# Performance work log

Measured on AMD Instinct MI355X. Metric: run time of the kernel, lower is better.

The kernel has to match this reference:

```python
import jax, jax.numpy as jnp
import numpy as np

W_L1, W_NORMAL, W_LAPLACIAN = 1.0, 1.0, 0.1
NORM_EPS = 1e-6   # F.normalize eps
COS_EPS = 1e-8    # F.cosine_similarity default eps


def setup_inputs() -> dict:
    key = jax.random.key(0)
    k1, k2, k3, k4, k5, k6 = jax.random.split(key, 6)
    N, F, NNZ = 1_000_000, 2_000_000, 8_000_000
    return {
        "V_rec": jax.random.normal(k1, (N, 3), dtype=jnp.float32),
        "V_gt": jax.random.normal(k2, (N, 3), dtype=jnp.float32),
        "faces": jax.random.randint(k3, (F, 3), 0, N, dtype=jnp.int64)
        if jax.config.jax_enable_x64 else jax.random.randint(k3, (F, 3), 0, N, dtype=jnp.int32),
        "L_rows": jax.random.randint(k4, (NNZ,), 0, N, dtype=jnp.int32),
        "L_cols": jax.random.randint(k5, (NNZ,), 0, N, dtype=jnp.int32),
        "L_vals": jax.random.normal(k6, (NNZ,), dtype=jnp.float32),
    }


def _vertex_normals(verts, faces):
    # gather verts by face indices: [F,3] each
    v0 = verts[faces[:, 0]]
    v1 = verts[faces[:, 1]]
    v2 = verts[faces[:, 2]]
    face_normals = jnp.cross(v1 - v0, v2 - v0)  # [F,3]
    vn = (jnp.zeros_like(verts)
          .at[faces[:, 0]].add(face_normals)
          .at[faces[:, 1]].add(face_normals)
          .at[faces[:, 2]].add(face_normals))
    norm = jnp.linalg.norm(vn, axis=1, keepdims=True)
    return vn / jnp.maximum(norm, NORM_EPS)


def _cosine_sim(a, b):
    dot = jnp.sum(a * b, axis=1)
    na = jnp.linalg.norm(a, axis=1)
    nb = jnp.linalg.norm(b, axis=1)
    return dot / (jnp.maximum(na, COS_EPS) * jnp.maximum(nb, COS_EPS))


def _spmm(rows, cols, vals, V):
    # sparse [N,N] @ dense [N,3] via gather + segment_sum
    return jax.ops.segment_sum(vals[:, None] * V[cols], rows, num_segments=V.shape[0])


def reference(V_rec, V_gt, faces, L_rows, L_cols, L_vals):
    # L1 term
    loss_l1 = jnp.mean(jnp.abs(V_rec - V_gt))
    # Normal cosine term
    normals_gt = _vertex_normals(V_gt, faces)
    normals_rec = _vertex_normals(V_rec, faces)
    cos_n = jnp.nan_to_num(_cosine_sim(normals_rec, normals_gt), nan=1.0)
    loss_normal = jnp.mean(1.0 - cos_n)
    # Laplacian cosine term
    delta_gt = _spmm(L_rows, L_cols, L_vals, V_gt)
    delta_rec = _spmm(L_rows, L_cols, L_vals, V_rec)
    cos_l = jnp.nan_to_num(_cosine_sim(delta_rec, delta_gt), nan=1.0)
    loss_laplacian = jnp.mean(1.0 - cos_l)
    finite = jnp.isfinite(delta_gt).all() & jnp.isfinite(delta_rec).all()
    loss_laplacian = jnp.where(finite, loss_laplacian, 0.0)
    return W_L1 * loss_l1 + W_NORMAL * loss_normal + W_LAPLACIAN * loss_laplacian
```

## Files before the change

### kernel.cpp

```cpp
#include <hip/hip_runtime.h>
#include <hip/hip_bf16.h>

#define NORM_EPS_F 1e-6f
#define COS_EPS_F  1e-8f
#define BK   512
#define BKSH 9
#define NBGMAX 2048
#define CHF1 2048
#define CHL1 4096
#define K2   32
#define NOCT 8

__device__ __forceinline__ void atomAddF(float* p, float v) {
    unsafeAtomicAdd(p, v);
}

template<int NV>
__device__ __forceinline__ void blockReduceAtomicN(float (&v)[NV], float* dst) {
    #pragma unroll
    for (int off = 32; off > 0; off >>= 1) {
        #pragma unroll
        for (int k = 0; k < NV; ++k) v[k] += __shfl_down(v[k], off, 64);
    }
    __shared__ float red[4][NV];
    int wave = threadIdx.x >> 6, lane = threadIdx.x & 63;
    if (lane == 0) {
        #pragma unroll
        for (int k = 0; k < NV; ++k) red[wave][k] = v[k];
    }
    __syncthreads();
    if (threadIdx.x == 0) {
        float s[NV];
        #pragma unroll
        for (int k = 0; k < NV; ++k) s[k] = 0.f;
        for (int w = 0; w < 4; ++w)
            #pragma unroll
            for (int k = 0; k < NV; ++k) s[k] += red[w][k];
        #pragma unroll
        for (int k = 0; k < NV; ++k) atomAddF(&dst[k], s[k]);
    }
}


__global__ void __launch_bounds__(256) pack_l1_kernel(
    const float* __restrict__ Vr, const float* __restrict__ Vg,
    float4* __restrict__ Vp, float* __restrict__ accum, int N)
{
    int i = blockIdx.x * blockDim.x + threadIdx.x;
    float l1[1] = {0.f};
    if (i < N) {
        float rx = Vr[3 * i], ry = Vr[3 * i + 1], rz = Vr[3 * i + 2];
        float gx = Vg[3 * i], gy = Vg[3 * i + 1], gz = Vg[3 * i + 2];
        Vp[2 * i]     = make_float4(rx, ry, rz, 0.f);
        Vp[2 * i + 1] = make_float4(gx, gy, gz, 0.f);
        l1[0] = fabsf(rx - gx) + fabsf(ry - gy) + fabsf(rz - gz);
    }
    blockReduceAtomicN<1>(l1, &accum[0]);
}

__global__ void __launch_bounds__(256) fn_kernel(
    const float4* __restrict__ Vp, const int* __restrict__ faces,
    float4* __restrict__ FN, int F)
{
    int half = (F + 1) >> 1;
    int t = blockIdx.x * blockDim.x + threadIdx.x;
    if (t >= half) return;
    int fi[2] = {t, t + half};
    int n = (fi[1] < F) ? 2 : 1;
    int idx[2][3];
    #pragma unroll
    for (int k = 0; k < 2; ++k) if (k < n) {
        idx[k][0] = faces[3 * fi[k]];
        idx[k][1] = faces[3 * fi[k] + 1];
        idx[k][2] = faces[3 * fi[k] + 2];
    }
    float4 r0[2], r1[2], r2[2], g0[2], g1[2], g2[2];
    #pragma unroll
    for (int k = 0; k < 2; ++k) if (k < n) {
        r0[k] = Vp[2 * idx[k][0]]; g0[k] = Vp[2 * idx[k][0] + 1];
        r1[k] = Vp[2 * idx[k][1]]; g1[k] = Vp[2 * idx[k][1] + 1];
        r2[k] = Vp[2 * idx[k][2]]; g2[k] = Vp[2 * idx[k][2] + 1];
    }
    #pragma unroll
    for (int k = 0; k < 2; ++k) if (k < n) {
        float ax = r1[k].x - r0[k].x, ay = r1[k].y - r0[k].y, az = r1[k].z - r0[k].z;
        float bx = r2[k].x - r0[k].x, by = r2[k].y - r0[k].y, bz = r2[k].z - r0[k].z;
        FN[2 * fi[k]] = make_float4(ay * bz - az * by, az * bx - ax * bz, ax * by - ay * bx, 0.f);
        ax = g1[k].x - g0[k].x; ay = g1[k].y - g0[k].y; az = g1[k].z - g0[k].z;
        bx = g2[k].x - g0[k].x; by = g2[k].y - g0[k].y; bz = g2[k].z - g0[k].z;
        FN[2 * fi[k] + 1] = make_float4(ay * bz - az * by, az * bx - ax * bz, ax * by - ay * bx, 0.f);
    }
}


__global__ void __launch_bounds__(256) bucket_F1(
    const int* __restrict__ faces, int* __restrict__ cntC,
    unsigned* __restrict__ recA, unsigned char* __restrict__ recC,
    int capC, int F, int b0, int bcnt, int chunk)
{
    __shared__ int hist[64];
    int f0 = blockIdx.x * chunk, f1 = min(f0 + chunk, F);
    if (threadIdx.x < 64) hist[threadIdx.x] = 0;
    __syncthreads();
    for (int f = f0 + threadIdx.x; f < f1; f += 256) {
        #pragma unroll
        for (int c = 0; c < 3; ++c) {
            unsigned fb = ((unsigned)faces[3 * f + c] >> BKSH) - (unsigned)b0;
            if (fb < (unsigned)bcnt) atomicAdd(&hist[fb >> 5], 1);
        }
    }
    __syncthreads();
    if (threadIdx.x < 64) {
        int h = hist[threadIdx.x];
        if (h) hist[threadIdx.x] = atomicAdd(&cntC[threadIdx.x], h);
    }
    __syncthreads();
    for (int f = f0 + threadIdx.x; f < f1; f += 256) {
        #pragma unroll
        for (int c = 0; c < 3; ++c) {
            int v = faces[3 * f + c];
            unsigned fb = ((unsigned)v >> BKSH) - (unsigned)b0;
            if (fb < (unsigned)bcnt) {
                int pos = atomicAdd(&hist[fb >> 5], 1);
                if (pos < capC) {
                    size_t idx = (size_t)(fb >> 5) * capC + pos;
                    recA[idx] = ((unsigned)f << BKSH) | ((unsigned)v & (BK - 1));
                    recC[idx] = (unsigned char)(fb & 31);
                }
            }
        }
    }
}

__global__ void __launch_bounds__(256) bucket_L1(
    const int* __restrict__ rows, const int* __restrict__ cols,
    const float* __restrict__ vals, int* __restrict__ cntC,
    int2* __restrict__ recA, unsigned char* __restrict__ recC,
    int capC, int nnz, int b0, int bcnt, int chunk, int octsh)
{
    __shared__ int hist[64];
    int i0 = blockIdx.x * chunk, i1 = min(i0 + chunk, nnz);
    if (threadIdx.x < 64) hist[threadIdx.x] = 0;
    __syncthreads();
    for (int i = i0 + threadIdx.x; i < i1; i += 256) {
        unsigned fb = ((unsigned)rows[i] >> BKSH) - (unsigned)b0;
        if (fb < (unsigned)bcnt) atomicAdd(&hist[fb >> 5], 1);
    }
    __syncthreads();
    if (threadIdx.x < 64) {
        int h = hist[threadIdx.x];
        if (h) hist[threadIdx.x] = atomicAdd(&cntC[threadIdx.x], h);
    }
    __syncthreads();
    for (int i = i0 + threadIdx.x; i < i1; i += 256) {
        int r = rows[i];
        unsigned fb = ((unsigned)r >> BKSH) - (unsigned)b0;
        if (fb < (unsigned)bcnt) {
            int pos = atomicAdd(&hist[fb >> 5], 1);
            if (pos < capC) {
                size_t idx = (size_t)(fb >> 5) * capC + pos;
                unsigned c = (unsigned)cols[i];
                recA[idx] = make_int2(
                    (int)((c << BKSH) | ((unsigned)r & (BK - 1))),
                    __float_as_int(vals[i]));
                recC[idx] = (unsigned char)(((fb & 31) << 3) | (c >> octsh));
            }
        }
    }
}


__global__ void __launch_bounds__(256) bucket_F2(
    const int* __restrict__ cntC, const unsigned* __restrict__ recA,
    const unsigned char* __restrict__ recC, int capC,
    int* __restrict__ cntFine, unsigned* __restrict__ fine, int capF)
{
    __shared__ int hist[32];
    int c = blockIdx.x;
    int K = gridDim.y, k = blockIdx.y;
    int ch = (capC + K - 1) / K;
    int n = min(cntC[c], capC);
    int i0 = k * ch, i1 = min(i0 + ch, n);
    if (threadIdx.x < 32) hist[threadIdx.x] = 0;
    __syncthreads();
    const size_t base = (size_t)c * capC;
    for (int i = i0 + threadIdx.x; i < i1; i += 256)
        atomicAdd(&hist[recC[base + i]], 1);
    __syncthreads();
    if (threadIdx.x < 32) {
        int h = hist[threadIdx.x];
        if (h) hist[threadIdx.x] = atomicAdd(&cntFine[(c << 5) + threadIdx.x], h);
    }
    __syncthreads();
    for (int i = i0 + threadIdx.x; i < i1; i += 256) {
        int fic = recC[base + i];
        int pos = atomicAdd(&hist[fic], 1);
        if (pos < capF)
            fine[(size_t)((c << 5) + fic) * capF + pos] = recA[base + i];
    }
}

__global__ void __launch_bounds__(256) bucket_L2(
    const int* __restrict__ cntC, const int2* __restrict__ recA,
    const unsigned char* __restrict__ recC, int capC,
    int* __restrict__ cntFine, int2* __restrict__ fine, int capS)
{
    __shared__ int hist[256];
    int c = blockIdx.x;
    int K = gridDim.y, k = blockIdx.y;
    int ch = (capC + K - 1) / K;
    int n = min(cntC[c], capC);
    int i0 = k * ch, i1 = min(i0 + ch, n);
    hist[threadIdx.x] = 0;
    __syncthreads();
    const size_t base = (size_t)c * capC;
    for (int i = i0 + threadIdx.x; i < i1; i += 256)
        atomicAdd(&hist[recC[base + i]], 1);
    __syncthreads();
    {
        int h = hist[threadIdx.x];
        if (h) hist[threadIdx.x] = atomicAdd(&cntFine[(c << 8) + threadIdx.x], h);
    }
    __syncthreads();
    for (int i = i0 + threadIdx.x; i < i1; i += 256) {
        int fic = recC[base + i];
        int pos = atomicAdd(&hist[fic], 1);
        if (pos < capS)
            fine[(size_t)((c << 8) + fic) * capS + pos] = recA[base + i];
    }
}


__global__ void __launch_bounds__(256) accum_normals_kernel(
    const float4* __restrict__ Vp, const float4* __restrict__ FN,
    const int* __restrict__ faces,
    const int* __restrict__ cnt, const unsigned* __restrict__ recF, int capF,
    float* __restrict__ accum, int N, int b0, int use_fn)
{
    __shared__ float vnr[3 * BK];
    __shared__ float vng[3 * BK];
    int g = blockIdx.x;
    for (int i = threadIdx.x; i < 3 * BK; i += blockDim.x) { vnr[i] = 0.f; vng[i] = 0.f; }
    __syncthreads();

    const unsigned* rec = recF + (size_t)g * capF;
    int n = min(cnt[g], capF);
    int i = threadIdx.x;
    if (use_fn) {
        for (; i + 768 < n; i += 1024) {
            unsigned rc[4];
            rc[0] = rec[i]; rc[1] = rec[i + 256]; rc[2] = rec[i + 512]; rc[3] = rec[i + 768];
            float4 nr[4], ng[4];
            #pragma unroll
            for (int k = 0; k < 4; ++k) {
                int f = rc[k] >> BKSH;
                nr[k] = FN[2 * f];
                ng[k] = FN[2 * f + 1];
            }
            #pragma unroll
            for (int k = 0; k < 4; ++k) {
                int lv = rc[k] & (BK - 1);
                atomicAdd(&vnr[3 * lv + 0], nr[k].x);
                atomicAdd(&vnr[3 * lv + 1], nr[k].y);
                atomicAdd(&vnr[3 * lv + 2], nr[k].z);
                atomicAdd(&vng[3 * lv + 0], ng[k].x);
                atomicAdd(&vng[3 * lv + 1], ng[k].y);
                atomicAdd(&vng[3 * lv + 2], ng[k].z);
            }
        }
    }
    for (; i < n; i += 256) {
        unsigned rc = rec[i];
        int lv = rc & (BK - 1);
        int f  = rc >> BKSH;
        float4 nr, ng;
        if (use_fn) {
            nr = FN[2 * f];
            ng = FN[2 * f + 1];
        } else {
            int i0 = faces[3 * f], i1 = faces[3 * f + 1], i2 = faces[3 * f + 2];
            float4 r0 = Vp[2 * i0], r1 = Vp[2 * i1], r2 = Vp[2 * i2];
            float4 g0 = Vp[2 * i0 + 1], g1 = Vp[2 * i1 + 1], g2 = Vp[2 * i2 + 1];
            float ax = r1.x - r0.x, ay = r1.y - r0.y, az = r1.z - r0.z;
            float bx = r2.x - r0.x, by = r2.y - r0.y, bz = r2.z - r0.z;
            nr = make_float4(ay * bz - az * by, az * bx - ax * bz, ax * by - ay * bx, 0.f);
            ax = g1.x - g0.x; ay = g1.y - g0.y; az = g1.z - g0.z;
            bx = g2.x - g0.x; by = g2.y - g0.y; bz = g2.z - g0.z;
            ng = make_float4(ay * bz - az * by, az * bx - ax * bz, ax * by - ay * bx, 0.f);
        }
        atomicAdd(&vnr[3 * lv + 0], nr.x);
        atomicAdd(&vnr[3 * lv + 1], nr.y);
        atomicAdd(&vnr[3 * lv + 2], nr.z);
        atomicAdd(&vng[3 * lv + 0], ng.x);
        atomicAdd(&vng[3 * lv + 1], ng.y);
        atomicAdd(&vng[3 * lv + 2], ng.z);
    }
    __syncthreads();

    float ln[1] = {0.f};
    for (int lv = threadIdx.x; lv < BK; lv += blockDim.x) {
        int gv = ((b0 + g) << BKSH) + lv;
        if (gv < N) {
            float ax = vnr[3 * lv], ay = vnr[3 * lv + 1], az = vnr[3 * lv + 2];
            float bx = vng[3 * lv], by = vng[3 * lv + 1], bz = vng[3 * lv + 2];
            float na = sqrtf(ax * ax + ay * ay + az * az);
            float nb = sqrtf(bx * bx + by * by + bz * bz);
            float ia = 1.0f / fmaxf(na, NORM_EPS_F);
            float ib = 1.0f / fmaxf(nb, NORM_EPS_F);
            ax *= ia; ay *= ia; az *= ia;
            bx *= ib; by *= ib; bz *= ib;
            float dot = ax * bx + ay * by + az * bz;
            float nna = sqrtf(ax * ax + ay * ay + az * az);
            float nnb = sqrtf(bx * bx + by * by + bz * bz);
            float cosn = dot / (fmaxf(nna, COS_EPS_F) * fmaxf(nnb, COS_EPS_F));
            if (isnan(cosn)) cosn = 1.0f;
            ln[0] += 1.0f - cosn;
        }
    }
    blockReduceAtomicN<1>(ln, &accum[1]);
}

__global__ void __launch_bounds__(256) accum_lap_kernel(
    const float4* __restrict__ Vp,
    const int* __restrict__ cntFine, const int2* __restrict__ recL, int capS,
    float* __restrict__ accum, int N, int b0)
{
    __shared__ float dlr[3 * BK];
    __shared__ float dlg[3 * BK];
    int g = blockIdx.x;
    for (int i = threadIdx.x; i < 3 * BK; i += blockDim.x) { dlr[i] = 0.f; dlg[i] = 0.f; }
    __syncthreads();

    for (int oct = 0; oct < NOCT; ++oct) {
        const int2* rec = recL + ((size_t)g * NOCT + oct) * capS;
        int n = min(cntFine[g * NOCT + oct], capS);
        int i = threadIdx.x;
        for (; i + 256 < n; i += 512) {
            int2 rc0 = rec[i], rc1 = rec[i + 256];
            int c0 = (unsigned)rc0.x >> BKSH, c1 = (unsigned)rc1.x >> BKSH;
            float4 pr0 = Vp[2 * c0], pg0 = Vp[2 * c0 + 1];
            float4 pr1 = Vp[2 * c1], pg1 = Vp[2 * c1 + 1];
            int lv0 = (unsigned)rc0.x & (BK - 1), lv1 = (unsigned)rc1.x & (BK - 1);
            float v0 = __int_as_float(rc0.y), v1 = __int_as_float(rc1.y);
            atomicAdd(&dlr[3 * lv0 + 0], v0 * pr0.x);
            atomicAdd(&dlr[3 * lv0 + 1], v0 * pr0.y);
            atomicAdd(&dlr[3 * lv0 + 2], v0 * pr0.z);
            atomicAdd(&dlg[3 * lv0 + 0], v0 * pg0.x);
            atomicAdd(&dlg[3 * lv0 + 1], v0 * pg0.y);
            atomicAdd(&dlg[3 * lv0 + 2], v0 * pg0.z);
            atomicAdd(&dlr[3 * lv1 + 0], v1 * pr1.x);
            atomicAdd(&dlr[3 * lv1 + 1], v1 * pr1.y);
            atomicAdd(&dlr[3 * lv1 + 2], v1 * pr1.z);
            atomicAdd(&dlg[3 * lv1 + 0], v1 * pg1.x);
            atomicAdd(&dlg[3 * lv1 + 1], v1 * pg1.y);
            atomicAdd(&dlg[3 * lv1 + 2], v1 * pg1.z);
        }
        for (; i < n; i += 256) {
            int2 rc = rec[i];
            unsigned u = (unsigned)rc.x;
            int lv  = u & (BK - 1);
            int col = u >> BKSH;
            float v = __int_as_float(rc.y);
            float4 pr = Vp[2 * col];
            float4 pg = Vp[2 * col + 1];
            atomicAdd(&dlr[3 * lv + 0], v * pr.x);
            atomicAdd(&dlr[3 * lv + 1], v * pr.y);
            atomicAdd(&dlr[3 * lv + 2], v * pr.z);
            atomicAdd(&dlg[3 * lv + 0], v * pg.x);
            atomicAdd(&dlg[3 * lv + 1], v * pg.y);
            atomicAdd(&dlg[3 * lv + 2], v * pg.z);
        }
    }
    __syncthreads();

    float vals2[2] = {0.f, 0.f};
    for (int lv = threadIdx.x; lv < BK; lv += blockDim.x) {
        int gv = ((b0 + g) << BKSH) + lv;
        if (gv < N) {
            float px = dlr[3 * lv], py = dlr[3 * lv + 1], pz = dlr[3 * lv + 2];
            float qx = dlg[3 * lv], qy = dlg[3 * lv + 1], qz = dlg[3 * lv + 2];
            bool fin = isfinite(px) && isfinite(py) && isfinite(pz) &&
                       isfinite(qx) && isfinite(qy) && isfinite(qz);
            vals2[1] += fin ? 0.f : 1.f;
            float dotl = px * qx + py * qy + pz * qz;
            float npn = sqrtf(px * px + py * py + pz * pz);
            float nqn = sqrtf(qx * qx + qy * qy + qz * qz);
            float cosl = dotl / (fmaxf(npn, COS_EPS_F) * fmaxf(nqn, COS_EPS_F));
            if (isnan(cosl)) cosl = 1.0f;
            vals2[0] += 1.0f - cosl;
        }
    }
    blockReduceAtomicN<2>(vals2, &accum[2]);
}

__global__ void finalize_kernel(const float* __restrict__ accum,
                                float* __restrict__ out, int N)
{
    float invN = 1.0f / (float)N;
    float l1 = accum[0] * invN * (1.0f / 3.0f);
    float ln = accum[1] * invN;
    float ll = (accum[3] > 0.0f) ? 0.0f : accum[2] * invN;
    out[0] = 1.0f * l1 + 1.0f * ln + 0.1f * ll;
}


__global__ void __launch_bounds__(256) face_normals_kernel(
    const float* __restrict__ Vr, const float* __restrict__ Vg,
    const int* __restrict__ faces,
    float* __restrict__ vn_rec, float* __restrict__ vn_gt, int F)
{
    int f = blockIdx.x * blockDim.x + threadIdx.x;
    if (f >= F) return;
    int i0 = faces[3 * f + 0], i1 = faces[3 * f + 1], i2 = faces[3 * f + 2];
    {
        float v0x = Vr[3 * i0], v0y = Vr[3 * i0 + 1], v0z = Vr[3 * i0 + 2];
        float v1x = Vr[3 * i1], v1y = Vr[3 * i1 + 1], v1z = Vr[3 * i1 + 2];
        float v2x = Vr[3 * i2], v2y = Vr[3 * i2 + 1], v2z = Vr[3 * i2 + 2];
        float ax = v1x - v0x, ay = v1y - v0y, az = v1z - v0z;
        float bx = v2x - v0x, by = v2y - v0y, bz = v2z - v0z;
        float nx = ay * bz - az * by, ny = az * bx - ax * bz, nz = ax * by - ay * bx;
        atomAddF(&vn_rec[3 * i0], nx); atomAddF(&vn_rec[3 * i0 + 1], ny); atomAddF(&vn_rec[3 * i0 + 2], nz);
        atomAddF(&vn_rec[3 * i1], nx); atomAddF(&vn_rec[3 * i1 + 1], ny); atomAddF(&vn_rec[3 * i1 + 2], nz);
        atomAddF(&vn_rec[3 * i2], nx); atomAddF(&vn_rec[3 * i2 + 1], ny); atomAddF(&vn_rec[3 * i2 + 2], nz);
    }
    {
        float v0x = Vg[3 * i0], v0y = Vg[3 * i0 + 1], v0z = Vg[3 * i0 + 2];
        float v1x = Vg[3 * i1], v1y = Vg[3 * i1 + 1], v1z = Vg[3 * i1 + 2];
        float v2x = Vg[3 * i2], v2y = Vg[3 * i2 + 1], v2z = Vg[3 * i2 + 2];
        float ax = v1x - v0x, ay = v1y - v0y, az = v1z - v0z;
        float bx = v2x - v0x, by = v2y - v0y, bz = v2z - v0z;
        float nx = ay * bz - az * by, ny = az * bx - ax * bz, nz = ax * by - ay * bx;
        atomAddF(&vn_gt[3 * i0], nx); atomAddF(&vn_gt[3 * i0 + 1], ny); atomAddF(&vn_gt[3 * i0 + 2], nz);
        atomAddF(&vn_gt[3 * i1], nx); atomAddF(&vn_gt[3 * i1 + 1], ny); atomAddF(&vn_gt[3 * i1 + 2], nz);
        atomAddF(&vn_gt[3 * i2], nx); atomAddF(&vn_gt[3 * i2 + 1], ny); atomAddF(&vn_gt[3 * i2 + 2], nz);
    }
}

__global__ void __launch_bounds__(256) spmm_kernel(
    const float* __restrict__ Vr, const float* __restrict__ Vg,
    const int* __restrict__ rows, const int* __restrict__ cols,
    const float* __restrict__ vals,
    float* __restrict__ dl_rec, float* __restrict__ dl_gt, int nnz)
{
    int i = blockIdx.x * blockDim.x + threadIdx.x;
    if (i >= nnz) return;
    int r = rows[i], c = cols[i];
    float v = vals[i];
    atomAddF(&dl_rec[3 * r], v * Vr[3 * c]);
    atomAddF(&dl_rec[3 * r + 1], v * Vr[3 * c + 1]);
    atomAddF(&dl_rec[3 * r + 2], v * Vr[3 * c + 2]);
    atomAddF(&dl_gt[3 * r], v * Vg[3 * c]);
    atomAddF(&dl_gt[3 * r + 1], v * Vg[3 * c + 1]);
    atomAddF(&dl_gt[3 * r + 2], v * Vg[3 * c + 2]);
}

__global__ void __launch_bounds__(256) reduce_kernel(
    const float* __restrict__ Vr, const float* __restrict__ Vg,
    const float* __restrict__ vn_rec, const float* __restrict__ vn_gt,
    const float* __restrict__ dl_rec, const float* __restrict__ dl_gt,
    float* __restrict__ accum, int N)
{
    int i = blockIdx.x * blockDim.x + threadIdx.x;
    float l1 = 0.0f, ln = 0.0f, ll = 0.0f, nonfin = 0.0f;
    if (i < N) {
        float rx = Vr[3 * i], ry = Vr[3 * i + 1], rz = Vr[3 * i + 2];
        float gx = Vg[3 * i], gy = Vg[3 * i + 1], gz = Vg[3 * i + 2];
        l1 = fabsf(rx - gx) + fabsf(ry - gy) + fabsf(rz - gz);
        float ax = vn_rec[3 * i], ay = vn_rec[3 * i + 1], az = vn_rec[3 * i + 2];
        float bx = vn_gt[3 * i],  by = vn_gt[3 * i + 1],  bz = vn_gt[3 * i + 2];
        float na = sqrtf(ax * ax + ay * ay + az * az);
        float nb = sqrtf(bx * bx + by * by + bz * bz);
        float ia = 1.0f / fmaxf(na, NORM_EPS_F);
        float ib = 1.0f / fmaxf(nb, NORM_EPS_F);
        ax *= ia; ay *= ia; az *= ia; bx *= ib; by *= ib; bz *= ib;
        float dot = ax * bx + ay * by + az * bz;
        float nna = sqrtf(ax * ax + ay * ay + az * az);
        float nnb = sqrtf(bx * bx + by * by + bz * bz);
        float cosn = dot / (fmaxf(nna, COS_EPS_F) * fmaxf(nnb, COS_EPS_F));
        if (isnan(cosn)) cosn = 1.0f;
        ln = 1.0f - cosn;
        float px = dl_rec[3 * i], py = dl_rec[3 * i + 1], pz = dl_rec[3 * i + 2];
        float qx = dl_gt[3 * i],  qy = dl_gt[3 * i + 1],  qz = dl_gt[3 * i + 2];
        bool fin = isfinite(px) && isfinite(py) && isfinite(pz) &&
                   isfinite(qx) && isfinite(qy) && isfinite(qz);
        nonfin = fin ? 0.0f : 1.0f;
        float dotl = px * qx + py * qy + pz * qz;
        float npn = sqrtf(px * px + py * py + pz * pz);
        float nqn = sqrtf(qx * qx + qy * qy + qz * qz);
        float cosl = dotl / (fmaxf(npn, COS_EPS_F) * fmaxf(nqn, COS_EPS_F));
        if (isnan(cosl)) cosl = 1.0f;
        ll = 1.0f - cosl;
    }
    float a[1] = {l1};  blockReduceAtomicN<1>(a, &accum[0]);
    float b[1] = {ln};  blockReduceAtomicN<1>(b, &accum[1]);
    float c2[2] = {ll, nonfin}; blockReduceAtomicN<2>(c2, &accum[2]);
}


extern "C" void kernel_launch(void* const* d_in, const int* in_sizes, int n_in,
                              void* d_out, int out_size, void* d_ws, size_t ws_size,
                              hipStream_t stream)
{
    const float* Vr    = (const float*)d_in[0];
    const float* Vg    = (const float*)d_in[1];
    const int*   faces = (const int*)d_in[2];
    const int*   Lr    = (const int*)d_in[3];
    const int*   Lc    = (const int*)d_in[4];
    const float* Lv    = (const float*)d_in[5];

    const int N   = in_sizes[0] / 3;
    const int F   = in_sizes[2] / 3;
    const int NNZ = in_sizes[3];
    const int NB  = (N + BK - 1) >> BKSH;

    float* ws = (float*)d_ws;
    const int B = 256;

    int lg = 0;
    while ((1LL << lg) < N) ++lg;
    const int octsh = lg > 3 ? lg - 3 : 0;

    const long long totW   = (long long)(ws_size / 4);
    const long long fixedW = 4 + 64 + (long long)NBGMAX * NOCT;
    const long long vpW    = 8LL * N;
    const long long arenaW = totW - fixedW - vpW;
    const long long fnW    = 8LL * F;

    const int capF = 3 * F / (NB > 0 ? NB : 1) + 1 + 640;
    const int capL = NNZ / (NB > 0 ? NB : 1) + 1 + 640;
    const int capS = NNZ / ((NB > 0 ? NB : 1) * NOCT) + 1 + 256;

    auto fwords = [&](int nbg) -> long long {
        long long nc = (nbg + 31) / 32, capC = 32LL * capF;
        return nc * capC + (nc * capC + 3) / 4 + (long long)nbg * capF + 4;
    };
    auto lwords = [&](int nbg) -> long long {
        long long nc = (nbg + 31) / 32, capC = 32LL * capL;
        return nc * capC * 2 + (((nc * capC + 3) / 4 + 1) & ~1LL)
             + (long long)nbg * NOCT * capS * 2 + 4;
    };

    int NBG_F = NB < NBGMAX ? NB : NBGMAX;
    bool tierA = (arenaW - fnW) >= fwords(64);
    long long arenaF = tierA ? (arenaW - fnW) : arenaW;
    while (NBG_F > 64 && fwords(NBG_F) > arenaF) NBG_F -= 32;
    int NBG_L = NB < NBGMAX ? NB : NBGMAX;
    while (NBG_L > 64 && lwords(NBG_L) > arenaW) NBG_L -= 32;

    bool fast = (N <= (1 << 20)) && (F <= (1 << 22)) &&
                NBG_F >= 64 && NBG_L >= 64 &&
                fwords(NBG_F) <= arenaF && lwords(NBG_L) <= arenaW &&
                arenaW > 0;

    if (fast) {
        float*  accum   = ws;
        int*    cntC    = (int*)(ws + 4);
        int*    cntFine = (int*)(ws + 68);
        float4* Vp      = (float4*)(ws + fixedW);
        float*  arena   = ws + fixedW + vpW;

        const long long NCF = (NBG_F + 31) / 32, capCF = 32LL * capF;
        float4*        FN    = (float4*)arena;
        float*         fbase = tierA ? (arena + fnW) : arena;
        unsigned*      recAF = (unsigned*)fbase;
        unsigned char* recCF = (unsigned char*)(recAF + NCF * capCF);
        unsigned*      fineF = (unsigned*)(fbase + NCF * capCF + (NCF * capCF + 3) / 4);

        const long long NCL = (NBG_L + 31) / 32, capCL = 32LL * capL;
        int2*          recAL = (int2*)arena;
        unsigned char* recCL = (unsigned char*)(recAL + NCL * capCL);
        const long long bytesWL = ((NCL * capCL + 3) / 4 + 1) & ~1LL;
        int2*          fineL = (int2*)(arena + NCL * capCL * 2 + bytesWL);

        hipMemsetAsync(accum, 0, 4 * sizeof(float), stream);

        pack_l1_kernel<<<dim3((N + B - 1) / B), dim3(B), 0, stream>>>(Vr, Vg, Vp, accum, N);
        if (tierA) {
            int half = (F + 1) >> 1;
            fn_kernel<<<dim3((half + B - 1) / B), dim3(B), 0, stream>>>(Vp, faces, FN, F);
        }

        int passF = (NB + NBG_F - 1) / NBG_F;
        for (int p = 0; p < passF; ++p) {
            int b0 = p * NBG_F;
            int bcnt = NB - b0 < NBG_F ? NB - b0 : NBG_F;
            int nc = (bcnt + 31) / 32;
            hipMemsetAsync(ws + 4, 0, (64 + (size_t)NBGMAX) * sizeof(int), stream);
            bucket_F1<<<dim3((F + CHF1 - 1) / CHF1), dim3(B), 0, stream>>>(
                faces, cntC, recAF, recCF, (int)capCF, F, b0, bcnt, CHF1);
            bucket_F2<<<dim3(nc, K2), dim3(B), 0, stream>>>(
                cntC, recAF, recCF, (int)capCF, cntFine, fineF, capF);
            accum_normals_kernel<<<dim3(bcnt), dim3(B), 0, stream>>>(
                Vp, FN, faces, cntFine, fineF, capF, accum, N, b0, tierA ? 1 : 0);
        }

        int passL = (NB + NBG_L - 1) / NBG_L;
        for (int p = 0; p < passL; ++p) {
            int b0 = p * NBG_L;
            int bcnt = NB - b0 < NBG_L ? NB - b0 : NBG_L;
            int nc = (bcnt + 31) / 32;
            hipMemsetAsync(ws + 4, 0, (64 + (size_t)NBGMAX * NOCT) * sizeof(int), stream);
            bucket_L1<<<dim3((NNZ + CHL1 - 1) / CHL1), dim3(B), 0, stream>>>(
                Lr, Lc, Lv, cntC, recAL, recCL, (int)capCL, NNZ, b0, bcnt, CHL1, octsh);
            bucket_L2<<<dim3(nc, K2), dim3(B), 0, stream>>>(
                cntC, recAL, recCL, (int)capCL, cntFine, fineL, capS);
            accum_lap_kernel<<<dim3(bcnt), dim3(B), 0, stream>>>(
                Vp, cntFine, fineL, capS, accum, N, b0);
        }
        finalize_kernel<<<dim3(1), dim3(1), 0, stream>>>(accum, (float*)d_out, N);
    } else {
        float* vn_rec = ws;
        float* vn_gt  = ws + (size_t)3 * N;
        float* dl_rec = ws + (size_t)6 * N;
        float* dl_gt  = ws + (size_t)9 * N;
        float* accum  = ws + (size_t)12 * N;
        hipMemsetAsync(d_ws, 0, ((size_t)12 * N + 4) * sizeof(float), stream);
        face_normals_kernel<<<dim3((F + B - 1) / B), dim3(B), 0, stream>>>(Vr, Vg, faces, vn_rec, vn_gt, F);
        spmm_kernel<<<dim3((NNZ + B - 1) / B), dim3(B), 0, stream>>>(Vr, Vg, Lr, Lc, Lv, dl_rec, dl_gt, NNZ);
        reduce_kernel<<<dim3((N + B - 1) / B), dim3(B), 0, stream>>>(Vr, Vg, vn_rec, vn_gt, dl_rec, dl_gt, accum, N);
        finalize_kernel<<<dim3(1), dim3(1), 0, stream>>>(accum, (float*)d_out, N);
    }
}
```

Baseline: 1.144 ms.

## Pack face normals as fp16, sub-bucket faces by octant, grid-sync accumulation

```diff
diff --git a/kernel.cpp b/kernel.cpp
--- a/kernel.cpp
+++ b/kernel.cpp
@@ -1,5 +1,9 @@
 #include <hip/hip_runtime.h>
 #include <hip/hip_bf16.h>
+#include <hip/hip_fp16.h>
+#include <hip/hip_cooperative_groups.h>
+
+namespace cg = cooperative_groups;
 
 #define NORM_EPS_F 1e-6f
 #define COS_EPS_F  1e-8f
@@ -15,6 +19,17 @@
     unsafeAtomicAdd(p, v);
 }
 
+__device__ __forceinline__ unsigned packh2(float a, float b) {
+    return (unsigned)__half_as_ushort(__float2half(a)) |
+           ((unsigned)__half_as_ushort(__float2half(b)) << 16);
+}
+__device__ __forceinline__ float unpL(unsigned u) {
+    return __half2float(__ushort_as_half((unsigned short)(u & 0xffff)));
+}
+__device__ __forceinline__ float unpH(unsigned u) {
+    return __half2float(__ushort_as_half((unsigned short)(u >> 16)));
+}
+
 template<int NV>
 __device__ __forceinline__ void blockReduceAtomicN(float (&v)[NV], float* dst) {
     #pragma unroll
@@ -60,7 +75,7 @@
 
 __global__ void __launch_bounds__(256) fn_kernel(
     const float4* __restrict__ Vp, const int* __restrict__ faces,
-    float4* __restrict__ FN, int F)
+    uint4* __restrict__ FNH, int F)
 {
     int half = (F + 1) >> 1;
     int t = blockIdx.x * blockDim.x + threadIdx.x;
@@ -85,10 +100,11 @@
     for (int k = 0; k < 2; ++k) if (k < n) {
         float ax = r1[k].x - r0[k].x, ay = r1[k].y - r0[k].y, az = r1[k].z - r0[k].z;
         float bx = r2[k].x - r0[k].x, by = r2[k].y - r0[k].y, bz = r2[k].z - r0[k].z;
-        FN[2 * fi[k]] = make_float4(ay * bz - az * by, az * bx - ax * bz, ax * by - ay * bx, 0.f);
+        float nrx = ay * bz - az * by, nry = az * bx - ax * bz, nrz = ax * by - ay * bx;
         ax = g1[k].x - g0[k].x; ay = g1[k].y - g0[k].y; az = g1[k].z - g0[k].z;
         bx = g2[k].x - g0[k].x; by = g2[k].y - g0[k].y; bz = g2[k].z - g0[k].z;
-        FN[2 * fi[k] + 1] = make_float4(ay * bz - az * by, az * bx - ax * bz, ax * by - ay * bx, 0.f);
+        float ngx = ay * bz - az * by, ngy = az * bx - ax * bz, ngz = ax * by - ay * bx;
+        FNH[fi[k]] = make_uint4(packh2(nrx, nry), packh2(nrz, ngx), packh2(ngy, ngz), 0u);
     }
 }
 
@@ -96,7 +112,7 @@
 __global__ void __launch_bounds__(256) bucket_F1(
     const int* __restrict__ faces, int* __restrict__ cntC,
     unsigned* __restrict__ recA, unsigned char* __restrict__ recC,
-    int capC, int F, int b0, int bcnt, int chunk)
+    int capC, int F, int b0, int bcnt, int chunk, int fsh)
 {
     __shared__ int hist[64];
     int f0 = blockIdx.x * chunk, f1 = min(f0 + chunk, F);
@@ -125,7 +141,7 @@
                 if (pos < capC) {
                     size_t idx = (size_t)(fb >> 5) * capC + pos;
                     recA[idx] = ((unsigned)f << BKSH) | ((unsigned)v & (BK - 1));
-                    recC[idx] = (unsigned char)(fb & 31);
+                    recC[idx] = (unsigned char)(((fb & 31) << 3) | ((unsigned)f >> fsh));
                 }
             }
         }
@@ -173,37 +189,7 @@
 __global__ void __launch_bounds__(256) bucket_F2(
     const int* __restrict__ cntC, const unsigned* __restrict__ recA,
     const unsigned char* __restrict__ recC, int capC,
-    int* __restrict__ cntFine, unsigned* __restrict__ fine, int capF)
-{
-    __shared__ int hist[32];
-    int c = blockIdx.x;
-    int K = gridDim.y, k = blockIdx.y;
-    int ch = (capC + K - 1) / K;
-    int n = min(cntC[c], capC);
-    int i0 = k * ch, i1 = min(i0 + ch, n);
-    if (threadIdx.x < 32) hist[threadIdx.x] = 0;
-    __syncthreads();
-    const size_t base = (size_t)c * capC;
-    for (int i = i0 + threadIdx.x; i < i1; i += 256)
-        atomicAdd(&hist[recC[base + i]], 1);
-    __syncthreads();
-    if (threadIdx.x < 32) {
-        int h = hist[threadIdx.x];
-        if (h) hist[threadIdx.x] = atomicAdd(&cntFine[(c << 5) + threadIdx.x], h);
-    }
-    __syncthreads();
-    for (int i = i0 + threadIdx.x; i < i1; i += 256) {
-        int fic = recC[base + i];
-        int pos = atomicAdd(&hist[fic], 1);
-        if (pos < capF)
-            fine[(size_t)((c << 5) + fic) * capF + pos] = recA[base + i];
-    }
-}
-
-__global__ void __launch_bounds__(256) bucket_L2(
-    const int* __restrict__ cntC, const int2* __restrict__ recA,
-    const unsigned char* __restrict__ recC, int capC,
-    int* __restrict__ cntFine, int2* __restrict__ fine, int capS)
+    int* __restrict__ cntFine, unsigned* __restrict__ fine, int capFS)
 {
     __shared__ int hist[256];
     int c = blockIdx.x;
@@ -225,78 +211,83 @@
     for (int i = i0 + threadIdx.x; i < i1; i += 256) {
         int fic = recC[base + i];
         int pos = atomicAdd(&hist[fic], 1);
+        if (pos < capFS)
+            fine[(size_t)((c << 8) + fic) * capFS + pos] = recA[base + i];
+    }
+}
+
+__global__ void __launch_bounds__(256) bucket_L2(
+    const int* __restrict__ cntC, const int2* __restrict__ recA,
+    const unsigned char* __restrict__ recC, int capC,
+    int* __restrict__ cntFine, int2* __restrict__ fine, int capS)
+{
+    __shared__ int hist[256];
+    int c = blockIdx.x;
+    int K = gridDim.y, k = blockIdx.y;
+    int ch = (capC + K - 1) / K;
+    int n = min(cntC[c], capC);
+    int i0 = k * ch, i1 = min(i0 + ch, n);
+    hist[threadIdx.x] = 0;
+    __syncthreads();
+    const size_t base = (size_t)c * capC;
+    for (int i = i0 + threadIdx.x; i < i1; i += 256)
+        atomicAdd(&hist[recC[base + i]], 1);
+    __syncthreads();
+    {
+        int h = hist[threadIdx.x];
+        if (h) hist[threadIdx.x] = atomicAdd(&cntFine[(c << 8) + threadIdx.x], h);
+    }
+    __syncthreads();
+    for (int i = i0 + threadIdx.x; i < i1; i += 256) {
+        int fic = recC[base + i];
+        int pos = atomicAdd(&hist[fic], 1);
         if (pos < capS)
             fine[(size_t)((c << 8) + fic) * capS + pos] = recA[base + i];
     }
 }
 
 
-__global__ void __launch_bounds__(256) accum_normals_kernel(
-    const float4* __restrict__ Vp, const float4* __restrict__ FN,
-    const int* __restrict__ faces,
-    const int* __restrict__ cnt, const unsigned* __restrict__ recF, int capF,
-    float* __restrict__ accum, int N, int b0, int use_fn)
-{
-    __shared__ float vnr[3 * BK];
-    __shared__ float vng[3 * BK];
-    int g = blockIdx.x;
-    for (int i = threadIdx.x; i < 3 * BK; i += blockDim.x) { vnr[i] = 0.f; vng[i] = 0.f; }
-    __syncthreads();
-
-    const unsigned* rec = recF + (size_t)g * capF;
-    int n = min(cnt[g], capF);
+__device__ __forceinline__ void normals_accum_oct(
+    const uint4* __restrict__ FNH,
+    const unsigned* __restrict__ rec, int n,
+    float* vnr, float* vng)
+{
     int i = threadIdx.x;
-    if (use_fn) {
-        for (; i + 768 < n; i += 1024) {
-            unsigned rc[4];
-            rc[0] = rec[i]; rc[1] = rec[i + 256]; rc[2] = rec[i + 512]; rc[3] = rec[i + 768];
-            float4 nr[4], ng[4];
-            #pragma unroll
-            for (int k = 0; k < 4; ++k) {
-                int f = rc[k] >> BKSH;
-                nr[k] = FN[2 * f];
-                ng[k] = FN[2 * f + 1];
-            }
-            #pragma unroll
-            for (int k = 0; k < 4; ++k) {
-                int lv = rc[k] & (BK - 1);
-                atomicAdd(&vnr[3 * lv + 0], nr[k].x);
-                atomicAdd(&vnr[3 * lv + 1], nr[k].y);
-                atomicAdd(&vnr[3 * lv + 2], nr[k].z);
-                atomicAdd(&vng[3 * lv + 0], ng[k].x);
-                atomicAdd(&vng[3 * lv + 1], ng[k].y);
-                atomicAdd(&vng[3 * lv + 2], ng[k].z);
-            }
-        }
+    for (; i + 256 < n; i += 512) {
+        unsigned rc0 = rec[i], rc1 = rec[i + 256];
+        uint4 u0 = FNH[rc0 >> BKSH];
+        uint4 u1 = FNH[rc1 >> BKSH];
+        int lv0 = rc0 & (BK - 1), lv1 = rc1 & (BK - 1);
+        atomicAdd(&vnr[3 * lv0 + 0], unpL(u0.x));
+        atomicAdd(&vnr[3 * lv0 + 1], unpH(u0.x));
+        atomicAdd(&vnr[3 * lv0 + 2], unpL(u0.y));
+        atomicAdd(&vng[3 * lv0 + 0], unpH(u0.y));
+        atomicAdd(&vng[3 * lv0 + 1], unpL(u0.z));
+        atomicAdd(&vng[3 * lv0 + 2], unpH(u0.z));
+        atomicAdd(&vnr[3 * lv1 + 0], unpL(u1.x));
+        atomicAdd(&vnr[3 * lv1 + 1], unpH(u1.x));
+        atomicAdd(&vnr[3 * lv1 + 2], unpL(u1.y));
+        atomicAdd(&vng[3 * lv1 + 0], unpH(u1.y));
+        atomicAdd(&vng[3 * lv1 + 1], unpL(u1.z));
+        atomicAdd(&vng[3 * lv1 + 2], unpH(u1.z));
     }
     for (; i < n; i += 256) {
         unsigned rc = rec[i];
+        uint4 u = FNH[rc >> BKSH];
         int lv = rc & (BK - 1);
-        int f  = rc >> BKSH;
-        float4 nr, ng;
-        if (use_fn) {
-            nr = FN[2 * f];
-            ng = FN[2 * f + 1];
-        } else {
-            int i0 = faces[3 * f], i1 = faces[3 * f + 1], i2 = faces[3 * f + 2];
-            float4 r0 = Vp[2 * i0], r1 = Vp[2 * i1], r2 = Vp[2 * i2];
-            float4 g0 = Vp[2 * i0 + 1], g1 = Vp[2 * i1 + 1], g2 = Vp[2 * i2 + 1];
-            float ax = r1.x - r0.x, ay = r1.y - r0.y, az = r1.z - r0.z;
-            float bx = r2.x - r0.x, by = r2.y - r0.y, bz = r2.z - r0.z;
-            nr = make_float4(ay * bz - az * by, az * bx - ax * bz, ax * by - ay * bx, 0.f);
-            ax = g1.x - g0.x; ay = g1.y - g0.y; az = g1.z - g0.z;
-            bx = g2.x - g0.x; by = g2.y - g0.y; bz = g2.z - g0.z;
-            ng = make_float4(ay * bz - az * by, az * bx - ax * bz, ax * by - ay * bx, 0.f);
-        }
-        atomicAdd(&vnr[3 * lv + 0], nr.x);
-        atomicAdd(&vnr[3 * lv + 1], nr.y);
-        atomicAdd(&vnr[3 * lv + 2], nr.z);
-        atomicAdd(&vng[3 * lv + 0], ng.x);
-        atomicAdd(&vng[3 * lv + 1], ng.y);
-        atomicAdd(&vng[3 * lv + 2], ng.z);
-    }
-    __syncthreads();
-
+        atomicAdd(&vnr[3 * lv + 0], unpL(u.x));
+        atomicAdd(&vnr[3 * lv + 1], unpH(u.x));
+        atomicAdd(&vnr[3 * lv + 2], unpL(u.y));
+        atomicAdd(&vng[3 * lv + 0], unpH(u.y));
+        atomicAdd(&vng[3 * lv + 1], unpL(u.z));
+        atomicAdd(&vng[3 * lv + 2], unpH(u.z));
+    }
+}
+
+__device__ __forceinline__ void normals_epilogue(
+    const float* vnr, const float* vng,
+    float* accum, int N, int b0, int g)
+{
     float ln[1] = {0.f};
     for (int lv = threadIdx.x; lv < BK; lv += blockDim.x) {
         int gv = ((b0 + g) << BKSH) + lv;
@@ -320,59 +311,115 @@
     blockReduceAtomicN<1>(ln, &accum[1]);
 }
 
-__global__ void __launch_bounds__(256) accum_lap_kernel(
+__global__ void __launch_bounds__(256) accum_normals_coop(
+    const uint4* __restrict__ FNH,
+    const int* __restrict__ cntFine, const unsigned* __restrict__ recF, int capFS,
+    float* __restrict__ accum, int N, int b0)
+{
+    __shared__ float vnr[3 * BK];
+    __shared__ float vng[3 * BK];
+    int g = blockIdx.x;
+    for (int i = threadIdx.x; i < 3 * BK; i += blockDim.x) { vnr[i] = 0.f; vng[i] = 0.f; }
+    __syncthreads();
+    for (int oct = 0; oct < NOCT; ++oct) {
+        if (oct) cg::this_grid().sync();
+        const unsigned* rec = recF + ((size_t)g * NOCT + oct) * capFS;
+        int n = min(cntFine[g * NOCT + oct], capFS);
+        normals_accum_oct(FNH, rec, n, vnr, vng);
+    }
+    __syncthreads();
+    normals_epilogue(vnr, vng, accum, N, b0, g);
+}
+
+__global__ void __launch_bounds__(256) accum_normals_legacy(
+    const float4* __restrict__ Vp, const uint4* __restrict__ FNH,
+    const int* __restrict__ faces,
+    const int* __restrict__ cntFine, const unsigned* __restrict__ recF, int capFS,
+    float* __restrict__ accum, int N, int b0, int use_fn)
+{
+    __shared__ float vnr[3 * BK];
+    __shared__ float vng[3 * BK];
+    int g = blockIdx.x;
+    for (int i = threadIdx.x; i < 3 * BK; i += blockDim.x) { vnr[i] = 0.f; vng[i] = 0.f; }
+    __syncthreads();
+    for (int oct = 0; oct < NOCT; ++oct) {
+        const unsigned* rec = recF + ((size_t)g * NOCT + oct) * capFS;
+        int n = min(cntFine[g * NOCT + oct], capFS);
+        if (use_fn) {
+            normals_accum_oct(FNH, rec, n, vnr, vng);
+        } else {
+            for (int i = threadIdx.x; i < n; i += 256) {
+                unsigned rc = rec[i];
+                int lv = rc & (BK - 1);
+                int f  = rc >> BKSH;
+                int i0 = faces[3 * f], i1 = faces[3 * f + 1], i2 = faces[3 * f + 2];
+                float4 r0 = Vp[2 * i0], r1 = Vp[2 * i1], r2 = Vp[2 * i2];
+                float4 g0 = Vp[2 * i0 + 1], g1 = Vp[2 * i1 + 1], g2 = Vp[2 * i2 + 1];
+                float ax = r1.x - r0.x, ay = r1.y - r0.y, az = r1.z - r0.z;
+                float bx = r2.x - r0.x, by = r2.y - r0.y, bz = r2.z - r0.z;
+                atomicAdd(&vnr[3 * lv + 0], ay * bz - az * by);
+                atomicAdd(&vnr[3 * lv + 1], az * bx - ax * bz);
+                atomicAdd(&vnr[3 * lv + 2], ax * by - ay * bx);
+                ax = g1.x - g0.x; ay = g1.y - g0.y; az = g1.z - g0.z;
+                bx = g2.x - g0.x; by = g2.y - g0.y; bz = g2.z - g0.z;
+                atomicAdd(&vng[3 * lv + 0], ay * bz - az * by);
+                atomicAdd(&vng[3 * lv + 1], az * bx - ax * bz);
+                atomicAdd(&vng[3 * lv + 2], ax * by - ay * bx);
+            }
+        }
+    }
+    __syncthreads();
+    normals_epilogue(vnr, vng, accum, N, b0, g);
+}
+
+
+__device__ __forceinline__ void lap_accum_oct(
     const float4* __restrict__ Vp,
-    const int* __restrict__ cntFine, const int2* __restrict__ recL, int capS,
-    float* __restrict__ accum, int N, int b0)
-{
-    __shared__ float dlr[3 * BK];
-    __shared__ float dlg[3 * BK];
-    int g = blockIdx.x;
-    for (int i = threadIdx.x; i < 3 * BK; i += blockDim.x) { dlr[i] = 0.f; dlg[i] = 0.f; }
-    __syncthreads();
-
-    for (int oct = 0; oct < NOCT; ++oct) {
-        const int2* rec = recL + ((size_t)g * NOCT + oct) * capS;
-        int n = min(cntFine[g * NOCT + oct], capS);
-        int i = threadIdx.x;
-        for (; i + 256 < n; i += 512) {
-            int2 rc0 = rec[i], rc1 = rec[i + 256];
-            int c0 = (unsigned)rc0.x >> BKSH, c1 = (unsigned)rc1.x >> BKSH;
-            float4 pr0 = Vp[2 * c0], pg0 = Vp[2 * c0 + 1];
-            float4 pr1 = Vp[2 * c1], pg1 = Vp[2 * c1 + 1];
-            int lv0 = (unsigned)rc0.x & (BK - 1), lv1 = (unsigned)rc1.x & (BK - 1);
-            float v0 = __int_as_float(rc0.y), v1 = __int_as_float(rc1.y);
-            atomicAdd(&dlr[3 * lv0 + 0], v0 * pr0.x);
-            atomicAdd(&dlr[3 * lv0 + 1], v0 * pr0.y);
-            atomicAdd(&dlr[3 * lv0 + 2], v0 * pr0.z);
-            atomicAdd(&dlg[3 * lv0 + 0], v0 * pg0.x);
-            atomicAdd(&dlg[3 * lv0 + 1], v0 * pg0.y);
-            atomicAdd(&dlg[3 * lv0 + 2], v0 * pg0.z);
-            atomicAdd(&dlr[3 * lv1 + 0], v1 * pr1.x);
-            atomicAdd(&dlr[3 * lv1 + 1], v1 * pr1.y);
-            atomicAdd(&dlr[3 * lv1 + 2], v1 * pr1.z);
-            atomicAdd(&dlg[3 * lv1 + 0], v1 * pg1.x);
-            atomicAdd(&dlg[3 * lv1 + 1], v1 * pg1.y);
-            atomicAdd(&dlg[3 * lv1 + 2], v1 * pg1.z);
-        }
-        for (; i < n; i += 256) {
-            int2 rc = rec[i];
-            unsigned u = (unsigned)rc.x;
-            int lv  = u & (BK - 1);
-            int col = u >> BKSH;
-            float v = __int_as_float(rc.y);
-            float4 pr = Vp[2 * col];
-            float4 pg = Vp[2 * col + 1];
-            atomicAdd(&dlr[3 * lv + 0], v * pr.x);
-            atomicAdd(&dlr[3 * lv + 1], v * pr.y);
-            atomicAdd(&dlr[3 * lv + 2], v * pr.z);
-            atomicAdd(&dlg[3 * lv + 0], v * pg.x);
-            atomicAdd(&dlg[3 * lv + 1], v * pg.y);
-            atomicAdd(&dlg[3 * lv + 2], v * pg.z);
-        }
-    }
-    __syncthreads();
-
+    const int2* __restrict__ rec, int n,
+    float* dlr, float* dlg)
+{
+    int i = threadIdx.x;
+    for (; i + 256 < n; i += 512) {
+        int2 rc0 = rec[i], rc1 = rec[i + 256];
+        int c0 = (unsigned)rc0.x >> BKSH, c1 = (unsigned)rc1.x >> BKSH;
+        float4 pr0 = Vp[2 * c0], pg0 = Vp[2 * c0 + 1];
+        float4 pr1 = Vp[2 * c1], pg1 = Vp[2 * c1 + 1];
+        int lv0 = (unsigned)rc0.x & (BK - 1), lv1 = (unsigned)rc1.x & (BK - 1);
+        float v0 = __int_as_float(rc0.y), v1 = __int_as_float(rc1.y);
+        atomicAdd(&dlr[3 * lv0 + 0], v0 * pr0.x);
+        atomicAdd(&dlr[3 * lv0 + 1], v0 * pr0.y);
+        atomicAdd(&dlr[3 * lv0 + 2], v0 * pr0.z);
+        atomicAdd(&dlg[3 * lv0 + 0], v0 * pg0.x);
+        atomicAdd(&dlg[3 * lv0 + 1], v0 * pg0.y);
+        atomicAdd(&dlg[3 * lv0 + 2], v0 * pg0.z);
+        atomicAdd(&dlr[3 * lv1 + 0], v1 * pr1.x);
+        atomicAdd(&dlr[3 * lv1 + 1], v1 * pr1.y);
+        atomicAdd(&dlr[3 * lv1 + 2], v1 * pr1.z);
+        atomicAdd(&dlg[3 * lv1 + 0], v1 * pg1.x);
+        atomicAdd(&dlg[3 * lv1 + 1], v1 * pg1.y);
+        atomicAdd(&dlg[3 * lv1 + 2], v1 * pg1.z);
+    }
+    for (; i < n; i += 256) {
+        int2 rc = rec[i];
+        unsigned u = (unsigned)rc.x;
+        int lv  = u & (BK - 1);
+        int col = u >> BKSH;
+        float v = __int_as_float(rc.y);
+        float4 pr = Vp[2 * col];
+        float4 pg = Vp[2 * col + 1];
+        atomicAdd(&dlr[3 * lv + 0], v * pr.x);
+        atomicAdd(&dlr[3 * lv + 1], v * pr.y);
+        atomicAdd(&dlr[3 * lv + 2], v * pr.z);
+        atomicAdd(&dlg[3 * lv + 0], v * pg.x);
+        atomicAdd(&dlg[3 * lv + 1], v * pg.y);
+        atomicAdd(&dlg[3 * lv + 2], v * pg.z);
+    }
+}
+
+__device__ __forceinline__ void lap_epilogue(
+    const float* dlr, const float* dlg,
+    float* accum, int N, int b0, int g)
+{
     float vals2[2] = {0.f, 0.f};
     for (int lv = threadIdx.x; lv < BK; lv += blockDim.x) {
         int gv = ((b0 + g) << BKSH) + lv;
@@ -391,6 +438,45 @@
         }
     }
     blockReduceAtomicN<2>(vals2, &accum[2]);
+}
+
+__global__ void __launch_bounds__(256) accum_lap_coop(
+    const float4* __restrict__ Vp,
+    const int* __restrict__ cntFine, const int2* __restrict__ recL, int capS,
+    float* __restrict__ accum, int N, int b0)
+{
+    __shared__ float dlr[3 * BK];
+    __shared__ float dlg[3 * BK];
+    int g = blockIdx.x;
+    for (int i = threadIdx.x; i < 3 * BK; i += blockDim.x) { dlr[i] = 0.f; dlg[i] = 0.f; }
+    __syncthreads();
+    for (int oct = 0; oct < NOCT; ++oct) {
+        if (oct) cg::this_grid().sync();
+        const int2* rec = recL + ((size_t)g * NOCT + oct) * capS;
+        int n = min(cntFine[g * NOCT + oct], capS);
+        lap_accum_oct(Vp, rec, n, dlr, dlg);
+    }
+    __syncthreads();
+    lap_epilogue(dlr, dlg, accum, N, b0, g);
+}
+
+__global__ void __launch_bounds__(256) accum_lap_legacy(
+    const float4* __restrict__ Vp,
+    const int* __restrict__ cntFine, const int2* __restrict__ recL, int capS,
+    float* __restrict__ accum, int N, int b0)
+{
+    __shared__ float dlr[3 * BK];
+    __shared__ float dlg[3 * BK];
+    int g = blockIdx.x;
+    for (int i = threadIdx.x; i < 3 * BK; i += blockDim.x) { dlr[i] = 0.f; dlg[i] = 0.f; }
+    __syncthreads();
+    for (int oct = 0; oct < NOCT; ++oct) {
+        const int2* rec = recL + ((size_t)g * NOCT + oct) * capS;
+        int n = min(cntFine[g * NOCT + oct], capS);
+        lap_accum_oct(Vp, rec, n, dlr, dlg);
+    }
+    __syncthreads();
+    lap_epilogue(dlr, dlg, accum, N, b0, g);
 }
 
 __global__ void finalize_kernel(const float* __restrict__ accum,
@@ -516,23 +602,25 @@
     float* ws = (float*)d_ws;
     const int B = 256;
 
-    int lg = 0;
-    while ((1LL << lg) < N) ++lg;
-    const int octsh = lg > 3 ? lg - 3 : 0;
+    int lgN = 0; while ((1LL << lgN) < N) ++lgN;
+    const int octsh = lgN > 3 ? lgN - 3 : 0;
+    int lgF = 0; while ((1LL << lgF) < F) ++lgF;
+    const int fsh = lgF > 3 ? lgF - 3 : 0;
 
     const long long totW   = (long long)(ws_size / 4);
     const long long fixedW = 4 + 64 + (long long)NBGMAX * NOCT;
     const long long vpW    = 8LL * N;
     const long long arenaW = totW - fixedW - vpW;
-    const long long fnW    = 8LL * F;
-
-    const int capF = 3 * F / (NB > 0 ? NB : 1) + 1 + 640;
-    const int capL = NNZ / (NB > 0 ? NB : 1) + 1 + 640;
-    const int capS = NNZ / ((NB > 0 ? NB : 1) * NOCT) + 1 + 256;
+    const long long fnW    = 4LL * F;
+
+    const int capF  = 3 * F / (NB > 0 ? NB : 1) + 1 + 640;
+    const int capL  = NNZ / (NB > 0 ? NB : 1) + 1 + 640;
+    const int capFS = 3 * F / ((NB > 0 ? NB : 1) * NOCT) + 1 + 256;
+    const int capS  = NNZ / ((NB > 0 ? NB : 1) * NOCT) + 1 + 256;
 
     auto fwords = [&](int nbg) -> long long {
         long long nc = (nbg + 31) / 32, capC = 32LL * capF;
-        return nc * capC + (nc * capC + 3) / 4 + (long long)nbg * capF + 4;
+        return nc * capC + (nc * capC + 3) / 4 + (long long)nbg * NOCT * capFS + 4;
     };
     auto lwords = [&](int nbg) -> long long {
         long long nc = (nbg + 31) / 32, capC = 32LL * capL;
@@ -560,7 +648,7 @@
         float*  arena   = ws + fixedW + vpW;
 
         const long long NCF = (NBG_F + 31) / 32, capCF = 32LL * capF;
-        float4*        FN    = (float4*)arena;
+        uint4*         FNH   = (uint4*)arena;
         float*         fbase = tierA ? (arena + fnW) : arena;
         unsigned*      recAF = (unsigned*)fbase;
         unsigned char* recCF = (unsigned char*)(recAF + NCF * capCF);
@@ -572,12 +660,23 @@
         const long long bytesWL = ((NCL * capCL + 3) / 4 + 1) & ~1LL;
         int2*          fineL = (int2*)(arena + NCL * capCL * 2 + bytesWL);
 
+        int dev = 0; hipGetDevice(&dev);
+        int numCU = 256;
+        hipDeviceGetAttribute(&numCU, hipDeviceAttributeMultiprocessorCount, dev);
+        int mbL = 0, mbN = 0;
+        hipOccupancyMaxActiveBlocksPerMultiprocessor(&mbL, accum_lap_coop, 256, 0);
+        hipOccupancyMaxActiveBlocksPerMultiprocessor(&mbN, accum_normals_coop, 256, 0);
+        int bcntF0 = NB < NBG_F ? NB : NBG_F;
+        int bcntL0 = NB < NBG_L ? NB : NBG_L;
+        bool coopN = tierA && ((long long)mbN * numCU >= bcntF0);
+        bool coopL = ((long long)mbL * numCU >= bcntL0);
+
         hipMemsetAsync(accum, 0, 4 * sizeof(float), stream);
 
         pack_l1_kernel<<<dim3((N + B - 1) / B), dim3(B), 0, stream>>>(Vr, Vg, Vp, accum, N);
         if (tierA) {
             int half = (F + 1) >> 1;
-            fn_kernel<<<dim3((half + B - 1) / B), dim3(B), 0, stream>>>(Vp, faces, FN, F);
+            fn_kernel<<<dim3((half + B - 1) / B), dim3(B), 0, stream>>>(Vp, faces, FNH, F);
         }
 
         int passF = (NB + NBG_F - 1) / NBG_F;
@@ -585,13 +684,22 @@
             int b0 = p * NBG_F;
             int bcnt = NB - b0 < NBG_F ? NB - b0 : NBG_F;
             int nc = (bcnt + 31) / 32;
-            hipMemsetAsync(ws + 4, 0, (64 + (size_t)NBGMAX) * sizeof(int), stream);
+            hipMemsetAsync(ws + 4, 0, (64 + (size_t)NBGMAX * NOCT) * sizeof(int), stream);
             bucket_F1<<<dim3((F + CHF1 - 1) / CHF1), dim3(B), 0, stream>>>(
-                faces, cntC, recAF, recCF, (int)capCF, F, b0, bcnt, CHF1);
+                faces, cntC, recAF, recCF, (int)capCF, F, b0, bcnt, CHF1, fsh);
             bucket_F2<<<dim3(nc, K2), dim3(B), 0, stream>>>(
-                cntC, recAF, recCF, (int)capCF, cntFine, fineF, capF);
-            accum_normals_kernel<<<dim3(bcnt), dim3(B), 0, stream>>>(
-                Vp, FN, faces, cntFine, fineF, capF, accum, N, b0, tierA ? 1 : 0);
+                cntC, recAF, recCF, (int)capCF, cntFine, fineF, capFS);
+            if (coopN) {
+                const uint4* FNHc = FNH; const int* cfc = cntFine;
+                const unsigned* ffc = fineF; int capc = capFS;
+                float* acc = accum; int Nc = N, b0c = b0;
+                void* args[] = {&FNHc, &cfc, &ffc, &capc, &acc, &Nc, &b0c};
+                hipLaunchCooperativeKernel((void*)accum_normals_coop,
+                    dim3(bcnt), dim3(B), args, 0, stream);
+            } else {
+                accum_normals_legacy<<<dim3(bcnt), dim3(B), 0, stream>>>(
+                    Vp, FNH, faces, cntFine, fineF, capFS, accum, N, b0, tierA ? 1 : 0);
+            }
         }
 
         int passL = (NB + NBG_L - 1) / NBG_L;
@@ -604,8 +712,17 @@
                 Lr, Lc, Lv, cntC, recAL, recCL, (int)capCL, NNZ, b0, bcnt, CHL1, octsh);
             bucket_L2<<<dim3(nc, K2), dim3(B), 0, stream>>>(
                 cntC, recAL, recCL, (int)capCL, cntFine, fineL, capS);
-            accum_lap_kernel<<<dim3(bcnt), dim3(B), 0, stream>>>(
-                Vp, cntFine, fineL, capS, accum, N, b0);
+            if (coopL) {
+                const float4* Vpc = Vp; const int* cfc = cntFine;
+                const int2* flc = fineL; int capc = capS;
+                float* acc = accum; int Nc = N, b0c = b0;
+                void* args[] = {&Vpc, &cfc, &flc, &capc, &acc, &Nc, &b0c};
+                hipLaunchCooperativeKernel((void*)accum_lap_coop,
+                    dim3(bcnt), dim3(B), args, 0, stream);
+            } else {
+                accum_lap_legacy<<<dim3(bcnt), dim3(B), 0, stream>>>(
+                    Vp, cntFine, fineL, capS, accum, N, b0);
+            }
         }
         finalize_kernel<<<dim3(1), dim3(1), 0, stream>>>(accum, (float*)d_out, N);
     } else {
```

Result: slower. 4.097 ms (+258.3%).
